# Kernel optimization log

Hardware: AMD Instinct MI355X
Metric: run time of the kernel (lower is better)

The kernel has to match this reference:

```python
import jax, jax.numpy as jnp
import numpy as np
from jax import lax

SIGMAS = [0.5, 1.0, 2.0]
CHANNELS = 64

def _gaussian_kernel(sigma, channels):
    k = int(6 * sigma + 1) | 1
    x = np.arange(k, dtype=np.float32) - k // 2
    k1 = np.exp(-x ** 2 / (2 * sigma ** 2))
    k2 = np.outer(k1, k1)
    k2 = k2 / k2.sum()
    # depthwise weight layout OIHW with feature_group_count=channels: (C, 1, k, k)
    w = np.broadcast_to(k2[None, None], (channels, 1, k, k)).copy()
    return jnp.asarray(w)

_KERNELS = [_gaussian_kernel(s, CHANNELS) for s in SIGMAS]

def setup_inputs() -> dict:
    key = jax.random.key(0)
    k1, k2, k3 = jax.random.split(key, 3)
    x = jax.random.normal(k1, (8, CHANNELS, 256, 256), dtype=jnp.float32)
    fusion_w = jax.random.normal(k2, (CHANNELS, CHANNELS * len(SIGMAS)), dtype=jnp.float32) * 0.05
    fusion_b = jax.random.normal(k3, (CHANNELS,), dtype=jnp.float32) * 0.05
    return {"x": x, "fusion_w": fusion_w, "fusion_b": fusion_b}

def _depthwise(x, w):
    return lax.conv_general_dilated(
        x, w, window_strides=(1, 1), padding="SAME",
        dimension_numbers=("NCHW", "OIHW", "NCHW"),
        feature_group_count=x.shape[1])

def reference(x, fusion_w, fusion_b):
    # multi-scale depthwise Gaussian blurs, concat on channel dim
    multi_scale = jnp.concatenate([_depthwise(x, w) for w in _KERNELS], axis=1)  # [B, 3C, H, W]
    # 1x1 fusion conv + bias
    fused = jnp.einsum("bchw,oc->bohw", multi_scale, fusion_w) + fusion_b[None, :, None, None]
    return x + fused
```

## Files before the change

kernel.cpp:

```cpp
#include <hip/hip_runtime.h>
#include <hip/hip_bf16.h>
#include <math.h>

#define B_  8
#define C_  64
#define H_  256
#define W_  256
#define HW_ (H_*W_)
#define J_  192
#define TH_ 32

typedef __attribute__((ext_vector_type(8))) short short8;
typedef __attribute__((ext_vector_type(4))) float f32x4;

__device__ __forceinline__ ushort f2bf(float f) {
    union { float f; uint u; } v; v.f = f;
    uint u = v.u;
    return (ushort)((u + 0x7fffu + ((u >> 16) & 1u)) >> 16);
}
__device__ __forceinline__ float bf2f(ushort s) {
    union { uint u; float f; } v; v.u = ((uint)s) << 16;
    return v.f;
}
__device__ __forceinline__ uint pk(float a, float b) {
    return (uint)f2bf(a) | ((uint)f2bf(b) << 16);
}

__global__ __launch_bounds__(256) void k1_mix(
    const float* __restrict__ x, const float* __restrict__ fw,
    ushort* __restrict__ v)
{
    __shared__ ushort lxs[256 * 64];

    const int b      = blockIdx.x >> 8;
    const int pxbase = (blockIdx.x & 255) << 8;
    const int t      = threadIdx.x;
    const int lane   = t & 63;
    const int wv_    = t >> 6;

    {
        const int cg = lane;
        const float* xb = x + (size_t)b * C_ * HW_ + pxbase + 4 * cg;
#pragma unroll
        for (int i = 0; i < 4; ++i) {
            const int cb = wv_ * 4 + i * 16;
            const int c4 = wv_ + i * 4;
            float4 r0 = *(const float4*)(xb + (size_t)(cb + 0) * HW_);
            float4 r1 = *(const float4*)(xb + (size_t)(cb + 1) * HW_);
            float4 r2 = *(const float4*)(xb + (size_t)(cb + 2) * HW_);
            float4 r3 = *(const float4*)(xb + (size_t)(cb + 3) * HW_);
            const int sbase = c4 ^ (cg & 15);
            ushort* dst = &lxs[(4 * cg) * 64];
            *(uint2*)(dst + 0*64 + ((sbase ^ 0) * 4)) = make_uint2(pk(r0.x, r1.x), pk(r2.x, r3.x));
            *(uint2*)(dst + 1*64 + ((sbase ^ 4) * 4)) = make_uint2(pk(r0.y, r1.y), pk(r2.y, r3.y));
            *(uint2*)(dst + 2*64 + ((sbase ^ 8) * 4)) = make_uint2(pk(r0.z, r1.z), pk(r2.z, r3.z));
            *(uint2*)(dst + 3*64 + ((sbase ^ 12) * 4)) = make_uint2(pk(r0.w, r1.w), pk(r2.w, r3.w));
        }
    }

    const int n = lane & 15;
    const int q = lane >> 4;
    union Frag { short8 v; uint u[4]; };
    Frag wf[3][2];
#pragma unroll
    for (int i = 0; i < 3; ++i) {
        const int j  = (wv_ * 3 + i) * 16 + n;
        const float* wr = fw + (size_t)(j & 63) * J_ + (j >> 6) * 64;
#pragma unroll
        for (int kh = 0; kh < 2; ++kh) {
            float4 w0 = *(const float4*)(wr + kh * 32 + q * 8);
            float4 w1 = *(const float4*)(wr + kh * 32 + q * 8 + 4);
            wf[i][kh].u[0] = pk(w0.x, w0.y);
            wf[i][kh].u[1] = pk(w0.z, w0.w);
            wf[i][kh].u[2] = pk(w1.x, w1.y);
            wf[i][kh].u[3] = pk(w1.z, w1.w);
        }
    }

    __syncthreads();

    for (int mt = 0; mt < 16; ++mt) {
        const int px = mt * 16 + (lane & 15);
        const ushort* row = &lxs[px * 64];
        const int s = ((px >> 2) & 15) ^ ((px & 3) << 2);
        Frag a0, a1;
        {
            uint2 lo  = *(const uint2*)&row[((2*q    ) ^ s) * 4];
            uint2 hi  = *(const uint2*)&row[((2*q + 1) ^ s) * 4];
            a0.u[0] = lo.x;  a0.u[1] = lo.y;  a0.u[2] = hi.x;  a0.u[3] = hi.y;
            uint2 lo1 = *(const uint2*)&row[((8 + 2*q    ) ^ s) * 4];
            uint2 hi1 = *(const uint2*)&row[((8 + 2*q + 1) ^ s) * 4];
            a1.u[0] = lo1.x; a1.u[1] = lo1.y; a1.u[2] = hi1.x; a1.u[3] = hi1.y;
        }
#pragma unroll
        for (int i = 0; i < 3; ++i) {
            f32x4 acc = {0.f, 0.f, 0.f, 0.f};
            acc = __builtin_amdgcn_mfma_f32_16x16x32_bf16(a0.v, wf[i][0].v, acc, 0, 0, 0);
            acc = __builtin_amdgcn_mfma_f32_16x16x32_bf16(a1.v, wf[i][1].v, acc, 0, 0, 0);
            const int j   = (wv_ * 3 + i) * 16 + n;
            const int pxg = pxbase + mt * 16 + q * 4;
            *(uint2*)&v[(size_t)(b * J_ + j) * HW_ + pxg] =
                make_uint2(pk(acc[0], acc[1]), pk(acc[2], acc[3]));
        }
    }
}

struct Taps {
    float g0[5];
    float g1[7];
    float g2[13];
};

template<int R, int G>
__device__ __forceinline__ void blur_one(
    const ushort* __restrict__ vplane, const float* __restrict__ g,
    ushort* __restrict__ tmp, int h0, int cg, int rw, float4* acc)
{
    const int NR  = TH_ + 2 * R;
    const int K   = 2 * R + 1;
    const int NG  = 2 * G + 1;
    const int OFF = 4 * G - R;
    const int c0  = cg * 4;

    for (int row = rw; row < NR; row += 4) {
        const int gh = h0 - R + row;
        float o0 = 0.f, o1 = 0.f, o2 = 0.f, o3 = 0.f;
        if (gh >= 0 && gh < H_) {
            const ushort* vr = vplane + (size_t)gh * W_;
            float win[NG * 4];
#pragma unroll
            for (int gi = 0; gi < NG; ++gi) {
                const int gg = cg - G + gi;
                uint2 d = (gg >= 0 && gg < 64) ? *(const uint2*)(vr + gg * 4)
                                               : make_uint2(0u, 0u);
                win[gi*4+0] = bf2f((ushort)(d.x & 0xffffu));
                win[gi*4+1] = bf2f((ushort)(d.x >> 16));
                win[gi*4+2] = bf2f((ushort)(d.y & 0xffffu));
                win[gi*4+3] = bf2f((ushort)(d.y >> 16));
            }
#pragma unroll
            for (int dd = 0; dd < K; ++dd) {
                const float gd = g[dd];
                o0 += gd * win[OFF + dd + 0];
                o1 += gd * win[OFF + dd + 1];
                o2 += gd * win[OFF + dd + 2];
                o3 += gd * win[OFF + dd + 3];
            }
        }
        *(uint2*)&tmp[row * W_ + c0] = make_uint2(pk(o0, o1), pk(o2, o3));
    }
    __syncthreads();

    const int base = rw * 8;
#pragma unroll
    for (int k = 0; k < 8 + 2 * R; ++k) {
        uint2 raw = *(const uint2*)&tmp[(base + k) * W_ + c0];
        const float f0 = bf2f((ushort)(raw.x & 0xffffu));
        const float f1 = bf2f((ushort)(raw.x >> 16));
        const float f2 = bf2f((ushort)(raw.y & 0xffffu));
        const float f3 = bf2f((ushort)(raw.y >> 16));
        const int ilo = (k - 2 * R) > 0 ? (k - 2 * R) : 0;
        const int ihi = k < 7 ? k : 7;
#pragma unroll
        for (int i = ilo; i <= ihi; ++i) {
            const float gd = g[k - i];
            acc[i].x += gd * f0;
            acc[i].y += gd * f1;
            acc[i].z += gd * f2;
            acc[i].w += gd * f3;
        }
    }
    __syncthreads();
}

__global__ __launch_bounds__(256) void k2_blur(
    const ushort* __restrict__ v, const float* __restrict__ x,
    const float* __restrict__ bias, float* __restrict__ out,
    Taps taps)
{
    __shared__ ushort tmp[(TH_ + 12) * W_];

    const int t    = blockIdx.x;
    const int tile = t & 7;
    const int o    = (t >> 3) & 63;
    const int b    = t >> 9;
    const int h0   = tile * TH_;
    const int cg   = threadIdx.x & 63;
    const int rw   = threadIdx.x >> 6;
    const int c0   = cg * 4;

    float4 acc[TH_ / 4];
#pragma unroll
    for (int i = 0; i < TH_ / 4; ++i) acc[i] = make_float4(0.f, 0.f, 0.f, 0.f);

    const ushort* vp = v + (size_t)(b * J_ + o) * HW_;
    blur_one<2, 1>(vp,                       taps.g0, tmp, h0, cg, rw, acc);
    blur_one<3, 1>(vp + (size_t)C_ * HW_,    taps.g1, tmp, h0, cg, rw, acc);
    blur_one<6, 2>(vp + (size_t)(2*C_) * HW_, taps.g2, tmp, h0, cg, rw, acc);

    const float* xp = x   + ((size_t)b * C_ + o) * HW_ + (size_t)h0 * W_;
    float*       op = out + ((size_t)b * C_ + o) * HW_ + (size_t)h0 * W_;
    const float bo = bias[o];
#pragma unroll
    for (int i = 0; i < TH_ / 4; ++i) {
        const int row = rw * 8 + i;
        float4 xv = *(const float4*)&xp[(size_t)row * W_ + c0];
        float4 r;
        r.x = xv.x + bo + acc[i].x;
        r.y = xv.y + bo + acc[i].y;
        r.z = xv.z + bo + acc[i].z;
        r.w = xv.w + bo + acc[i].w;
        *(float4*)&op[(size_t)row * W_ + c0] = r;
    }
}

static void make_taps(Taps& t)
{
    auto fill = [](float* g, int k, double sigma) {
        int r = k / 2;
        double s = 0.0;
        for (int i = 0; i < k; ++i) {
            double w = exp(-(double)((i - r) * (i - r)) / (2.0 * sigma * sigma));
            g[i] = (float)w;
            s += w;
        }
        for (int i = 0; i < k; ++i) g[i] = (float)((double)g[i] / s);
    };
    fill(t.g0, 5, 0.5);
    fill(t.g1, 7, 1.0);
    fill(t.g2, 13, 2.0);
}

extern "C" void kernel_launch(void* const* d_in, const int* in_sizes, int n_in,
                              void* d_out, int out_size, void* d_ws, size_t ws_size,
                              hipStream_t stream)
{
    const float* x  = (const float*)d_in[0];
    const float* fw = (const float*)d_in[1];
    const float* fb = (const float*)d_in[2];
    float* out = (float*)d_out;
    ushort* v = (ushort*)d_ws;
    Taps taps;
    make_taps(taps);

    k1_mix<<<dim3(B_ * (HW_ / 256)), dim3(256), 0, stream>>>(x, fw, v);
    k2_blur<<<dim3(B_ * C_ * (H_ / TH_)), dim3(256), 0, stream>>>(v, x, fb, out, taps);
}
```

Measured before the change: 494.8 us.

## Drop shared-memory staging in blur; compute horizontal rows per-wave in registers

The blur kernel no longer stages horizontally blurred rows in LDS with block barriers. Each wave now recomputes its own 8+2R halo rows straight from global memory and feeds them into the vertical accumulators in registers. Gaussian taps become compile-time constants instead of a kernel argument, and the x loads in k1 are batched ahead of the bf16 packing. The aim is to remove the LDS traffic and the syncthreads, at the cost of redundant horizontal work and global reads for the overlapping halo rows between waves, plus more register pressure.

```diff
diff --git a/kernel.cpp b/kernel.cpp
--- a/kernel.cpp
+++ b/kernel.cpp
@@ -26,6 +26,17 @@
     return (uint)f2bf(a) | ((uint)f2bf(b) << 16);
 }
 
+constexpr float G0_[5]  = {2.6386598e-04f, 1.06450312e-01f, 7.86572828e-01f,
+                           1.06450312e-01f, 2.6386598e-04f};
+constexpr float G1_[7]  = {4.4330482e-03f, 5.40055826e-02f, 2.42036229e-01f,
+                           3.99050280e-01f, 2.42036229e-01f, 5.40055826e-02f,
+                           4.4330482e-03f};
+constexpr float G2_[13] = {2.2181980e-03f, 8.7731300e-03f, 2.7023161e-02f,
+                           6.4825174e-02f, 1.21109411e-01f, 1.76213165e-01f,
+                           1.99675640e-01f, 1.76213165e-01f, 1.21109411e-01f,
+                           6.4825174e-02f, 2.7023161e-02f, 8.7731300e-03f,
+                           2.2181980e-03f};
+
 __global__ __launch_bounds__(256) void k1_mix(
     const float* __restrict__ x, const float* __restrict__ fw,
     ushort* __restrict__ v)
@@ -41,14 +52,17 @@
     {
         const int cg = lane;
         const float* xb = x + (size_t)b * C_ * HW_ + pxbase + 4 * cg;
+        float4 r[16];
 #pragma unroll
         for (int i = 0; i < 4; ++i) {
-            const int cb = wv_ * 4 + i * 16;
+#pragma unroll
+            for (int rr = 0; rr < 4; ++rr)
+                r[i * 4 + rr] = *(const float4*)(xb + (size_t)(wv_ * 4 + i * 16 + rr) * HW_);
+        }
+#pragma unroll
+        for (int i = 0; i < 4; ++i) {
             const int c4 = wv_ + i * 4;
-            float4 r0 = *(const float4*)(xb + (size_t)(cb + 0) * HW_);
-            float4 r1 = *(const float4*)(xb + (size_t)(cb + 1) * HW_);
-            float4 r2 = *(const float4*)(xb + (size_t)(cb + 2) * HW_);
-            float4 r3 = *(const float4*)(xb + (size_t)(cb + 3) * HW_);
+            const float4 r0 = r[i*4+0], r1 = r[i*4+1], r2 = r[i*4+2], r3 = r[i*4+3];
             const int sbase = c4 ^ (cg & 15);
             ushort* dst = &lxs[(4 * cg) * 64];
             *(uint2*)(dst + 0*64 + ((sbase ^ 0) * 4)) = make_uint2(pk(r0.x, r1.x), pk(r2.x, r3.x));
@@ -105,33 +119,26 @@
     }
 }
 
-struct Taps {
-    float g0[5];
-    float g1[7];
-    float g2[13];
-};
-
 template<int R, int G>
-__device__ __forceinline__ void blur_one(
-    const ushort* __restrict__ vplane, const float* __restrict__ g,
-    ushort* __restrict__ tmp, int h0, int cg, int rw, float4* acc)
-{
-    const int NR  = TH_ + 2 * R;
-    const int K   = 2 * R + 1;
-    const int NG  = 2 * G + 1;
-    const int OFF = 4 * G - R;
-    const int c0  = cg * 4;
-
-    for (int row = rw; row < NR; row += 4) {
-        const int gh = h0 - R + row;
-        float o0 = 0.f, o1 = 0.f, o2 = 0.f, o3 = 0.f;
-        if (gh >= 0 && gh < H_) {
+__device__ __forceinline__ void blur_scale(
+    const ushort* __restrict__ vplane, const float (&g)[2 * R + 1],
+    int h0, int base, int cg, float4* acc)
+{
+    constexpr int NG  = 2 * G + 1;
+    constexpr int OFF = 4 * G - R;
+    constexpr int NK  = 8 + 2 * R;
+
+#pragma unroll
+    for (int k = 0; k < NK; ++k) {
+        const int gh = h0 + base - R + k;
+        float b0 = 0.f, b1 = 0.f, b2 = 0.f, b3 = 0.f;
+        if ((unsigned)gh < (unsigned)H_) {
             const ushort* vr = vplane + (size_t)gh * W_;
             float win[NG * 4];
 #pragma unroll
             for (int gi = 0; gi < NG; ++gi) {
                 const int gg = cg - G + gi;
-                uint2 d = (gg >= 0 && gg < 64) ? *(const uint2*)(vr + gg * 4)
+                uint2 d = ((unsigned)gg < 64u) ? *(const uint2*)(vr + gg * 4)
                                                : make_uint2(0u, 0u);
                 win[gi*4+0] = bf2f((ushort)(d.x & 0xffffu));
                 win[gi*4+1] = bf2f((ushort)(d.x >> 16));
@@ -139,47 +146,31 @@
                 win[gi*4+3] = bf2f((ushort)(d.y >> 16));
             }
 #pragma unroll
-            for (int dd = 0; dd < K; ++dd) {
-                const float gd = g[dd];
-                o0 += gd * win[OFF + dd + 0];
-                o1 += gd * win[OFF + dd + 1];
-                o2 += gd * win[OFF + dd + 2];
-                o3 += gd * win[OFF + dd + 3];
+            for (int d = 0; d <= 2 * R; ++d) {
+                const float gd = g[d];
+                b0 += gd * win[OFF + d + 0];
+                b1 += gd * win[OFF + d + 1];
+                b2 += gd * win[OFF + d + 2];
+                b3 += gd * win[OFF + d + 3];
             }
         }
-        *(uint2*)&tmp[row * W_ + c0] = make_uint2(pk(o0, o1), pk(o2, o3));
-    }
-    __syncthreads();
-
-    const int base = rw * 8;
-#pragma unroll
-    for (int k = 0; k < 8 + 2 * R; ++k) {
-        uint2 raw = *(const uint2*)&tmp[(base + k) * W_ + c0];
-        const float f0 = bf2f((ushort)(raw.x & 0xffffu));
-        const float f1 = bf2f((ushort)(raw.x >> 16));
-        const float f2 = bf2f((ushort)(raw.y & 0xffffu));
-        const float f3 = bf2f((ushort)(raw.y >> 16));
-        const int ilo = (k - 2 * R) > 0 ? (k - 2 * R) : 0;
-        const int ihi = k < 7 ? k : 7;
-#pragma unroll
-        for (int i = ilo; i <= ihi; ++i) {
-            const float gd = g[k - i];
-            acc[i].x += gd * f0;
-            acc[i].y += gd * f1;
-            acc[i].z += gd * f2;
-            acc[i].w += gd * f3;
-        }
-    }
-    __syncthreads();
+#pragma unroll
+        for (int i = 0; i < 8; ++i) {
+            if (k - i >= 0 && k - i <= 2 * R) {
+                const float gd = g[k - i];
+                acc[i].x += gd * b0;
+                acc[i].y += gd * b1;
+                acc[i].z += gd * b2;
+                acc[i].w += gd * b3;
+            }
+        }
+    }
 }
 
 __global__ __launch_bounds__(256) void k2_blur(
     const ushort* __restrict__ v, const float* __restrict__ x,
-    const float* __restrict__ bias, float* __restrict__ out,
-    Taps taps)
-{
-    __shared__ ushort tmp[(TH_ + 12) * W_];
-
+    const float* __restrict__ bias, float* __restrict__ out)
+{
     const int t    = blockIdx.x;
     const int tile = t & 7;
     const int o    = (t >> 3) & 63;
@@ -188,22 +179,23 @@
     const int cg   = threadIdx.x & 63;
     const int rw   = threadIdx.x >> 6;
     const int c0   = cg * 4;
-
-    float4 acc[TH_ / 4];
-#pragma unroll
-    for (int i = 0; i < TH_ / 4; ++i) acc[i] = make_float4(0.f, 0.f, 0.f, 0.f);
+    const int base = rw * 8;
+
+    float4 acc[8];
+#pragma unroll
+    for (int i = 0; i < 8; ++i) acc[i] = make_float4(0.f, 0.f, 0.f, 0.f);
 
     const ushort* vp = v + (size_t)(b * J_ + o) * HW_;
-    blur_one<2, 1>(vp,                       taps.g0, tmp, h0, cg, rw, acc);
-    blur_one<3, 1>(vp + (size_t)C_ * HW_,    taps.g1, tmp, h0, cg, rw, acc);
-    blur_one<6, 2>(vp + (size_t)(2*C_) * HW_, taps.g2, tmp, h0, cg, rw, acc);
+    blur_scale<2, 1>(vp,                        G0_, h0, base, cg, acc);
+    blur_scale<3, 1>(vp + (size_t)C_ * HW_,     G1_, h0, base, cg, acc);
+    blur_scale<6, 2>(vp + (size_t)(2*C_) * HW_, G2_, h0, base, cg, acc);
 
     const float* xp = x   + ((size_t)b * C_ + o) * HW_ + (size_t)h0 * W_;
     float*       op = out + ((size_t)b * C_ + o) * HW_ + (size_t)h0 * W_;
     const float bo = bias[o];
 #pragma unroll
-    for (int i = 0; i < TH_ / 4; ++i) {
-        const int row = rw * 8 + i;
+    for (int i = 0; i < 8; ++i) {
+        const int row = base + i;
         float4 xv = *(const float4*)&xp[(size_t)row * W_ + c0];
         float4 r;
         r.x = xv.x + bo + acc[i].x;
@@ -214,23 +206,6 @@
     }
 }
 
-static void make_taps(Taps& t)
-{
-    auto fill = [](float* g, int k, double sigma) {
-        int r = k / 2;
-        double s = 0.0;
-        for (int i = 0; i < k; ++i) {
-            double w = exp(-(double)((i - r) * (i - r)) / (2.0 * sigma * sigma));
-            g[i] = (float)w;
-            s += w;
-        }
-        for (int i = 0; i < k; ++i) g[i] = (float)((double)g[i] / s);
-    };
-    fill(t.g0, 5, 0.5);
-    fill(t.g1, 7, 1.0);
-    fill(t.g2, 13, 2.0);
-}
-
 extern "C" void kernel_launch(void* const* d_in, const int* in_sizes, int n_in,
                               void* d_out, int out_size, void* d_ws, size_t ws_size,
                               hipStream_t stream)
@@ -240,9 +215,7 @@
     const float* fb = (const float*)d_in[2];
     float* out = (float*)d_out;
     ushort* v = (ushort*)d_ws;
-    Taps taps;
-    make_taps(taps);
 
     k1_mix<<<dim3(B_ * (HW_ / 256)), dim3(256), 0, stream>>>(x, fw, v);
-    k2_blur<<<dim3(B_ * C_ * (H_ / TH_)), dim3(256), 0, stream>>>(v, x, fb, out, taps);
-}
+    k2_blur<<<dim3(B_ * C_ * (H_ / TH_)), dim3(256), 0, stream>>>(v, x, fb, out);
+}
```

Result: slower. 600.6 us (+21.4%).
